# Optimization experiments

Hardware: AMD Instinct MI355X
Metric: run time of the kernel (lower is better)

Reference implementation:

```python
import jax, jax.numpy as jnp
import numpy as np

B, S, D = 2, 2048, 768
H = 12
HD = D // H  # 64
SCALE = HD ** -0.5


def setup_inputs() -> dict:
    key = jax.random.key(0)
    k1, k2, k3, k4, k5 = jax.random.split(key, 5)
    x = jax.random.normal(k1, (B, S, D), dtype=jnp.float32)
    w_qkv = jax.random.normal(k2, (D, 3 * D), dtype=jnp.float32) * (D ** -0.5)
    b_qkv = jax.random.normal(k3, (3 * D,), dtype=jnp.float32) * 0.02
    w_proj = jax.random.normal(k4, (D, D), dtype=jnp.float32) * (D ** -0.5)
    b_proj = jax.random.normal(k5, (D,), dtype=jnp.float32) * 0.02
    return {"x": x, "w_qkv": w_qkv, "b_qkv": b_qkv, "w_proj": w_proj, "b_proj": b_proj}


def reference(x, w_qkv, b_qkv, w_proj, b_proj):
    b, s, d = x.shape
    # QKV projection: (B,S,3D) -> (3,B,H,S,HD)
    qkv = x @ w_qkv + b_qkv
    qkv = qkv.reshape(b, s, 3, H, HD).transpose(2, 0, 3, 1, 4)
    q, k, v = qkv[0], qkv[1], qkv[2]
    q = q * SCALE
    # full NxN attention scores, as in the original module
    attn = jnp.einsum("bhqd,bhkd->bhqk", q, k)
    attn = jax.nn.softmax(attn, axis=-1)
    out = jnp.einsum("bhqk,bhkd->bhqd", attn, v)  # (B,H,S,HD)
    out = out.transpose(0, 2, 1, 3).reshape(b, s, d)
    return out @ w_proj + b_proj
```

## Files before the change

### kernel.cpp

```cpp
#include <hip/hip_runtime.h>
#include <hip/hip_bf16.h>

#define B_ 2
#define S_ 2048
#define D_ 768
#define H_ 12
#define HD_ 64
#define EXP2C_ 0.1803368801111244f

typedef __attribute__((ext_vector_type(8))) short bf16x8;
typedef __attribute__((ext_vector_type(8))) unsigned short u16x8;
typedef __attribute__((ext_vector_type(4))) float f32x4;
typedef __attribute__((ext_vector_type(4))) unsigned int u32x4;

static __device__ __forceinline__ unsigned short f2bf(float x) {
    union { float f; unsigned u; } v; v.f = x;
    unsigned r = (v.u + 0x7FFFu + ((v.u >> 16) & 1u)) >> 16;
    return (unsigned short)r;
}
static __device__ __forceinline__ float bf2f(unsigned short h) {
    union { unsigned u; float f; } v; v.u = ((unsigned)h) << 16;
    return v.f;
}
static __device__ __forceinline__ float fexp2(float x) { return __builtin_exp2f(x); }

static __device__ __forceinline__ unsigned pk_bf16(float a, float b) {
    __hip_bfloat162 pk = __float22bfloat162_rn(make_float2(a, b));
    union { __hip_bfloat162 h; unsigned u; } v; v.h = pk;
    return v.u;
}

static __device__ __forceinline__ f32x4 mfma32(bf16x8 a, bf16x8 b, f32x4 c) {
    return __builtin_amdgcn_mfma_f32_16x16x32_bf16(a, b, c, 0, 0, 0);
}

typedef __attribute__((address_space(3))) unsigned int lds_u32;
typedef __attribute__((address_space(1))) const unsigned int glb_u32;
static __device__ __forceinline__ void glds16(const unsigned short* g, unsigned short* l) {
    __builtin_amdgcn_global_load_lds((glb_u32*)g, (lds_u32*)l, 16, 0, 0);
}

#define PREP_CONV_ 1536
#define PREP_TQKV_ 1728
#define PREP_TPRJ_ 576
__global__ __launch_bounds__(256) void prep_kernel(
    const float* __restrict__ x,      unsigned short* __restrict__ x16,
    const float* __restrict__ w_qkv,  unsigned short* __restrict__ wqkvT,
    const float* __restrict__ w_proj, unsigned short* __restrict__ wprojT)
{
    __shared__ float tile[32][33];
    const int bid = blockIdx.x, t = threadIdx.x;
    if (bid < PREP_CONV_) {
        const int i = (bid * 256 + t) * 8;
        float4 a0 = *(const float4*)(x + i);
        float4 a1 = *(const float4*)(x + i + 4);
        u16x8 s;
        s[0] = f2bf(a0.x); s[1] = f2bf(a0.y); s[2] = f2bf(a0.z); s[3] = f2bf(a0.w);
        s[4] = f2bf(a1.x); s[5] = f2bf(a1.y); s[6] = f2bf(a1.z); s[7] = f2bf(a1.w);
        *(u16x8*)(x16 + i) = s;
        return;
    }
    const float* w; unsigned short* wT; int N, bb;
    if (bid < PREP_CONV_ + PREP_TQKV_) { w = w_qkv; wT = wqkvT; N = 3 * D_; bb = bid - PREP_CONV_; }
    else                               { w = w_proj; wT = wprojT; N = D_;   bb = bid - PREP_CONV_ - PREP_TQKV_; }
    const int K = D_;
    const int nt = N / 32;
    const int n0 = (bb % nt) * 32, k0 = (bb / nt) * 32;
    const int tx = t & 31, ty = t >> 5;
#pragma unroll
    for (int i = 0; i < 4; i++)
        tile[ty + i * 8][tx] = w[(size_t)(k0 + ty + i * 8) * N + n0 + tx];
    __syncthreads();
#pragma unroll
    for (int i = 0; i < 4; i++)
        wT[(size_t)(n0 + ty + i * 8) * K + k0 + tx] = f2bf(tile[tx][ty + i * 8]);
}

template <int BM, int BN, bool OUT_F32>
__global__ __launch_bounds__(256) void gemm_bt_kernel(
    const unsigned short* __restrict__ A,
    const unsigned short* __restrict__ Bt,
    const float* __restrict__ bias,
    void* __restrict__ Cp,
    int M, int N, int K)
{
    __shared__ __align__(16) unsigned short As[BM][32];
    __shared__ __align__(16) unsigned short Bs[BN][32];
    constexpr int MI = BM / 32, NJ = BN / 32;
    constexpr int ACH = BM * 4, BCH = BN * 4;

    const int t = threadIdx.x;
    const int w = t >> 6, lane = t & 63, quad = lane >> 4, l16 = lane & 15;
    const int n0 = blockIdx.x * BN, m0 = blockIdx.y * BM;
    const int mw = (w & 1) * (BM / 2), nw = (w >> 1) * (BN / 2);

    const f32x4 z = {0.f, 0.f, 0.f, 0.f};
    f32x4 acc[MI][NJ];
#pragma unroll
    for (int i = 0; i < MI; i++)
#pragma unroll
        for (int j = 0; j < NJ; j++) acc[i][j] = z;

    for (int kk = 0; kk < K; kk += 32) {
#pragma unroll
        for (int it = 0; it < (ACH + 255) / 256; it++) {
            const int c = t + it * 256;
            if (ACH % 256 == 0 || c < ACH) {
                const int row = c >> 2, c8 = (c & 3) << 3;
                glds16(A + (size_t)(m0 + row) * K + kk + c8, &As[0][0] + c * 8);
            }
        }
#pragma unroll
        for (int it = 0; it < (BCH + 255) / 256; it++) {
            const int c = t + it * 256;
            if (BCH % 256 == 0 || c < BCH) {
                const int row = c >> 2, c8 = (c & 3) << 3;
                glds16(Bt + (size_t)(n0 + row) * K + kk + c8, &Bs[0][0] + c * 8);
            }
        }
        __syncthreads();

        bf16x8 a[MI], b[NJ];
#pragma unroll
        for (int i = 0; i < MI; i++)
            a[i] = *(const bf16x8*)(&As[mw + i * 16 + l16][quad * 8]);
#pragma unroll
        for (int j = 0; j < NJ; j++)
            b[j] = *(const bf16x8*)(&Bs[nw + j * 16 + l16][quad * 8]);
#pragma unroll
        for (int i = 0; i < MI; i++)
#pragma unroll
            for (int j = 0; j < NJ; j++)
                acc[i][j] = mfma32(a[i], b[j], acc[i][j]);
        __syncthreads();
    }

#pragma unroll
    for (int j = 0; j < NJ; j++) {
        const int col = n0 + nw + j * 16 + l16;
        const float bv = bias[col];
#pragma unroll
        for (int i = 0; i < MI; i++) {
#pragma unroll
            for (int r = 0; r < 4; r++) {
                const int row = m0 + mw + i * 16 + quad * 4 + r;
                const float v = acc[i][j][r] + bv;
                if (OUT_F32) ((float*)Cp)[(size_t)row * N + col] = v;
                else         ((unsigned short*)Cp)[(size_t)row * N + col] = f2bf(v);
            }
        }
    }
}

__global__ __launch_bounds__(256) void repack_v_kernel(
    const unsigned short* __restrict__ qkv,
    unsigned short* __restrict__ vt)
{
    __shared__ unsigned short T[64][65];
    const int t = threadIdx.x;
    const int bh = blockIdx.x, st = blockIdx.y;
    const int b = bh / H_, h = bh % H_;
    const unsigned short* src =
        qkv + (size_t)(b * S_ + st * 64) * (3 * D_) + 2 * D_ + h * HD_;

#pragma unroll
    for (int it = 0; it < 2; it++) {
        const int c = t + it * 256, sr = c >> 3, g = c & 7;
        u16x8 v = *(const u16x8*)(src + (size_t)sr * (3 * D_) + g * 8);
#pragma unroll
        for (int j = 0; j < 8; j++) T[sr][g * 8 + j] = v[j];
    }
    __syncthreads();
#pragma unroll
    for (int it = 0; it < 2; it++) {
        const int c = t + it * 256, hd = c >> 3, g = c & 7;
        u16x8 v;
#pragma unroll
        for (int j = 0; j < 8; j++) v[j] = T[g * 8 + j][hd];
        *(u16x8*)(vt + (size_t)(bh * HD_ + hd) * S_ + st * 64 + g * 8) = v;
    }
}

__global__ __launch_bounds__(256) void attn_kernel(
    const unsigned short* __restrict__ qkv,
    const unsigned short* __restrict__ vt,
    float* __restrict__ o_p0,
    float* __restrict__ o_p1,
    float* __restrict__ l_p)
{
    __shared__ __align__(16) unsigned short Ks[2][64][64];
    __shared__ __align__(16) unsigned short Vs[2][64][64];

    const int t = threadIdx.x;
    const int w = t >> 6, lane = t & 63, quad = lane >> 4, l16 = lane & 15;
    const int h8 = l16 & 7;
    const int qt = blockIdx.x, bh = blockIdx.y, ks = blockIdx.z;
    const int b = bh / H_, h = bh % H_;
    const int ld = 3 * D_;

    const unsigned short* qbase =
        qkv + (size_t)(b * S_ + qt * 64 + 16 * w + l16) * ld + h * HD_;
    u16x8 qr0 = *(const u16x8*)(qbase + quad * 8);
    u16x8 qr1 = *(const u16x8*)(qbase + 32 + quad * 8);
    bf16x8 qf0, qf1;
#pragma unroll
    for (int j = 0; j < 8; j++) {
        qf0[j] = (short)f2bf(bf2f(qr0[j]) * EXP2C_);
        qf1[j] = (short)f2bf(bf2f(qr1[j]) * EXP2C_);
    }

    bf16x8 ones;
#pragma unroll
    for (int j = 0; j < 8; j++) ones[j] = (short)0x3F80;

    const unsigned short* kbase =
        qkv + (size_t)(b * S_ + ks * 1024) * ld + D_ + h * HD_;
    const unsigned short* vbase = vt + (size_t)bh * HD_ * S_;

    const int c0 = t, c1 = t + 256;
    const int row0 = c0 >> 3, row1 = c1 >> 3;
    const int kg0 = (c0 & 7) ^ ((row0 & 3) | (((row0 >> 3) & 1) << 2));
    const int kg1 = (c1 & 7) ^ ((row1 & 3) | (((row1 >> 3) & 1) << 2));
    const int vg0 = (c0 & 7) ^ (row0 & 7);
    const int vg1 = (c1 & 7) ^ (row1 & 7);
    const unsigned short* kp0 = kbase + (size_t)row0 * ld + kg0 * 8;
    const unsigned short* kp1 = kbase + (size_t)row1 * ld + kg1 * 8;
    const unsigned short* vp0 = vbase + (size_t)row0 * S_ + ks * 1024 + vg0 * 8;
    const unsigned short* vp1 = vbase + (size_t)row1 * S_ + ks * 1024 + vg1 * 8;
    const size_t KSTEP = (size_t)64 * ld;

    const f32x4 z = {0.f, 0.f, 0.f, 0.f};
    f32x4 o_acc[4] = {z, z, z, z};
    f32x4 l_acc = z;

    glds16(kp0, &Ks[0][0][0] + c0 * 8);
    glds16(kp1, &Ks[0][0][0] + c1 * 8);
    glds16(vp0, &Vs[0][0][0] + c0 * 8);
    glds16(vp1, &Vs[0][0][0] + c1 * 8);
    kp0 += KSTEP; kp1 += KSTEP; vp0 += 64; vp1 += 64;
    __syncthreads();

    const int NT = 1024 / 64;
    for (int kt = 0; kt < NT; kt++) {
        const int buf = kt & 1;

        if (kt + 1 < NT) {
            unsigned short* kd = &Ks[buf ^ 1][0][0];
            unsigned short* vd = &Vs[buf ^ 1][0][0];
            glds16(kp0, kd + c0 * 8);
            glds16(kp1, kd + c1 * 8);
            glds16(vp0, vd + c0 * 8);
            glds16(vp1, vd + c1 * 8);
            kp0 += KSTEP; kp1 += KSTEP; vp0 += 64; vp1 += 64;
        }

        f32x4 s_acc[4] = {z, z, z, z};
#pragma unroll
        for (int nt = 0; nt < 4; nt++) {
            const int rowp = ((nt >> 1) << 5) + ((l16 >> 2) << 3) + ((nt & 1) << 2) + (l16 & 3);
            const int skr = (rowp & 3) | (((rowp >> 3) & 1) << 2);
            const unsigned short* kr = &Ks[buf][rowp][0];
            bf16x8 k0 = *(const bf16x8*)(kr + (quad ^ skr) * 8);
            bf16x8 k1 = *(const bf16x8*)(kr + ((quad ^ skr) ^ 4) * 8);
            s_acc[nt] = mfma32(k0, qf0, s_acc[nt]);
            s_acc[nt] = mfma32(k1, qf1, s_acc[nt]);
        }

        bf16x8 vr0[4], vr1[4];
#pragma unroll
        for (int nt = 0; nt < 4; nt++) {
            const int row = nt * 16 + l16;
            vr0[nt] = *(const bf16x8*)(&Vs[buf][row][(quad ^ h8) * 8]);
            vr1[nt] = *(const bf16x8*)(&Vs[buf][row][((quad ^ h8) ^ 4) * 8]);
        }

        f32x4 pr[4];
#pragma unroll
        for (int nt = 0; nt < 4; nt++) {
#pragma unroll
            for (int r = 0; r < 4; r++) pr[nt][r] = fexp2(s_acc[nt][r]);
        }
        union { u32x4 u; bf16x8 h; } ca, cb;
        ca.u[0] = pk_bf16(pr[0][0], pr[0][1]);
        ca.u[1] = pk_bf16(pr[0][2], pr[0][3]);
        ca.u[2] = pk_bf16(pr[1][0], pr[1][1]);
        ca.u[3] = pk_bf16(pr[1][2], pr[1][3]);
        cb.u[0] = pk_bf16(pr[2][0], pr[2][1]);
        cb.u[1] = pk_bf16(pr[2][2], pr[2][3]);
        cb.u[2] = pk_bf16(pr[3][0], pr[3][1]);
        cb.u[3] = pk_bf16(pr[3][2], pr[3][3]);
        const bf16x8 pa0 = ca.h, pa1 = cb.h;

        l_acc = mfma32(pa0, ones, l_acc);
        l_acc = mfma32(pa1, ones, l_acc);

#pragma unroll
        for (int nt = 0; nt < 4; nt++) {
            o_acc[nt] = mfma32(pa0, vr0[nt], o_acc[nt]);
            o_acc[nt] = mfma32(pa1, vr1[nt], o_acc[nt]);
        }

        __syncthreads();
    }

    float* op = ks ? o_p1 : o_p0;
    float* lp2 = l_p + (size_t)ks * (B_ * S_ * H_);
#pragma unroll
    for (int r = 0; r < 4; r++) {
        const int row = b * S_ + qt * 64 + 16 * w + quad * 4 + r;
        float* ob = op + (size_t)row * D_ + h * HD_;
#pragma unroll
        for (int nt = 0; nt < 4; nt++)
            ob[nt * 16 + l16] = o_acc[nt][r];
        if (l16 == 0) lp2[(size_t)row * H_ + h] = l_acc[r];
    }
}

__global__ __launch_bounds__(256) void combine_kernel(
    const float* __restrict__ o_p0,
    const float* __restrict__ o_p1,
    const float* __restrict__ l_p,
    unsigned short* __restrict__ o)
{
    const int i = (blockIdx.x * 256 + threadIdx.x) * 8;
    const int row = i / D_, col = i - row * D_, h = col >> 6;
    const float l0 = l_p[(size_t)row * H_ + h];
    const float l1 = l_p[(size_t)(B_ * S_ * H_) + row * H_ + h];
    const float inv = 1.f / (l0 + l1);
    float4 a0 = *(const float4*)(o_p0 + i);
    float4 a1 = *(const float4*)(o_p0 + i + 4);
    float4 b0 = *(const float4*)(o_p1 + i);
    float4 b1 = *(const float4*)(o_p1 + i + 4);
    u16x8 s;
    s[0] = f2bf((a0.x + b0.x) * inv); s[1] = f2bf((a0.y + b0.y) * inv);
    s[2] = f2bf((a0.z + b0.z) * inv); s[3] = f2bf((a0.w + b0.w) * inv);
    s[4] = f2bf((a1.x + b1.x) * inv); s[5] = f2bf((a1.y + b1.y) * inv);
    s[6] = f2bf((a1.z + b1.z) * inv); s[7] = f2bf((a1.w + b1.w) * inv);
    *(u16x8*)(o + i) = s;
}

extern "C" void kernel_launch(void* const* d_in, const int* in_sizes, int n_in,
                              void* d_out, int out_size, void* d_ws, size_t ws_size,
                              hipStream_t stream) {
    const float* x      = (const float*)d_in[0];
    const float* w_qkv  = (const float*)d_in[1];
    const float* b_qkv  = (const float*)d_in[2];
    const float* w_proj = (const float*)d_in[3];
    const float* b_proj = (const float*)d_in[4];
    float* out = (float*)d_out;

    unsigned short* qkv    = (unsigned short*)d_ws;
    unsigned short* vtb    = qkv    + (size_t)(B_ * S_) * (3 * D_);
    unsigned short* o_x16  = vtb    + (size_t)(B_ * H_) * HD_ * S_;
    unsigned short* wqkvT  = o_x16  + (size_t)(B_ * S_) * D_;
    unsigned short* wprojT = wqkvT  + (size_t)D_ * (3 * D_);
    float* o_p1 = (float*)(wprojT + (size_t)D_ * D_);
    float* l_p  = o_p1 + (size_t)(B_ * S_) * D_;
    float* o_p0 = out;

    dim3 blk(256);
    prep_kernel<<<dim3(PREP_CONV_ + PREP_TQKV_ + PREP_TPRJ_), blk, 0, stream>>>(
        x, o_x16, w_qkv, wqkvT, w_proj, wprojT);
    gemm_bt_kernel<128, 96, false><<<dim3((3 * D_) / 96, (B_ * S_) / 128), blk, 0, stream>>>(
        o_x16, wqkvT, b_qkv, qkv, B_ * S_, 3 * D_, D_);
    repack_v_kernel<<<dim3(B_ * H_, S_ / 64), blk, 0, stream>>>(qkv, vtb);
    attn_kernel<<<dim3(S_ / 64, B_ * H_, 2), blk, 0, stream>>>(qkv, vtb, o_p0, o_p1, l_p);
    combine_kernel<<<dim3((B_ * S_) * D_ / (256 * 8)), blk, 0, stream>>>(
        o_p0, o_p1, l_p, o_x16);
    gemm_bt_kernel<64, 64, true><<<dim3(D_ / 64, (B_ * S_) / 64), blk, 0, stream>>>(
        o_x16, wprojT, b_proj, out, B_ * S_, D_, D_);
}
```

Measured before the change: 176.3 us.

## Pre-swizzle V into MFMA fragment layout and load it directly to registers

The V-repack kernel now writes V in a layout that already matches the MFMA B-operand fragment order. The attention kernel then loads V fragments from global memory straight into registers, prefetched one tile ahead, and no longer stages them through a shared-memory double buffer. This halves LDS use and removes the LDS reads for V, and a launch-bounds hint asks for 5 blocks per CU. In exchange, every wave now reads V from global memory or cache independently instead of sharing one block load, and register pressure rises.

```diff
diff --git a/kernel.cpp b/kernel.cpp
--- a/kernel.cpp
+++ b/kernel.cpp
@@ -154,7 +154,7 @@
 
 __global__ __launch_bounds__(256) void repack_v_kernel(
     const unsigned short* __restrict__ qkv,
-    unsigned short* __restrict__ vt)
+    unsigned short* __restrict__ vtp)
 {
     __shared__ unsigned short T[64][65];
     const int t = threadIdx.x;
@@ -177,23 +177,23 @@
         u16x8 v;
 #pragma unroll
         for (int j = 0; j < 8; j++) v[j] = T[g * 8 + j][hd];
-        *(u16x8*)(vt + (size_t)(bh * HD_ + hd) * S_ + st * 64 + g * 8) = v;
-    }
-}
-
-__global__ __launch_bounds__(256) void attn_kernel(
+        const size_t off =
+            ((((size_t)(bh * 32 + st) * 4 + (hd >> 4)) * 8 + g) * 16 + (hd & 15)) * 8;
+        *(u16x8*)(vtp + off) = v;
+    }
+}
+
+__global__ __launch_bounds__(256, 5) void attn_kernel(
     const unsigned short* __restrict__ qkv,
-    const unsigned short* __restrict__ vt,
+    const unsigned short* __restrict__ vtp,
     float* __restrict__ o_p0,
     float* __restrict__ o_p1,
     float* __restrict__ l_p)
 {
     __shared__ __align__(16) unsigned short Ks[2][64][64];
-    __shared__ __align__(16) unsigned short Vs[2][64][64];
 
     const int t = threadIdx.x;
     const int w = t >> 6, lane = t & 63, quad = lane >> 4, l16 = lane & 15;
-    const int h8 = l16 & 7;
     const int qt = blockIdx.x, bh = blockIdx.y, ks = blockIdx.z;
     const int b = bh / H_, h = bh % H_;
     const int ld = 3 * D_;
@@ -215,18 +215,15 @@
 
     const unsigned short* kbase =
         qkv + (size_t)(b * S_ + ks * 1024) * ld + D_ + h * HD_;
-    const unsigned short* vbase = vt + (size_t)bh * HD_ * S_;
+    const unsigned short* vb =
+        vtp + ((size_t)bh * 32 + ks * 16) * 4096 + quad * 128 + l16 * 8;
 
     const int c0 = t, c1 = t + 256;
     const int row0 = c0 >> 3, row1 = c1 >> 3;
     const int kg0 = (c0 & 7) ^ ((row0 & 3) | (((row0 >> 3) & 1) << 2));
     const int kg1 = (c1 & 7) ^ ((row1 & 3) | (((row1 >> 3) & 1) << 2));
-    const int vg0 = (c0 & 7) ^ (row0 & 7);
-    const int vg1 = (c1 & 7) ^ (row1 & 7);
     const unsigned short* kp0 = kbase + (size_t)row0 * ld + kg0 * 8;
     const unsigned short* kp1 = kbase + (size_t)row1 * ld + kg1 * 8;
-    const unsigned short* vp0 = vbase + (size_t)row0 * S_ + ks * 1024 + vg0 * 8;
-    const unsigned short* vp1 = vbase + (size_t)row1 * S_ + ks * 1024 + vg1 * 8;
     const size_t KSTEP = (size_t)64 * ld;
 
     const f32x4 z = {0.f, 0.f, 0.f, 0.f};
@@ -235,23 +232,26 @@
 
     glds16(kp0, &Ks[0][0][0] + c0 * 8);
     glds16(kp1, &Ks[0][0][0] + c1 * 8);
-    glds16(vp0, &Vs[0][0][0] + c0 * 8);
-    glds16(vp1, &Vs[0][0][0] + c1 * 8);
-    kp0 += KSTEP; kp1 += KSTEP; vp0 += 64; vp1 += 64;
+    kp0 += KSTEP; kp1 += KSTEP;
+    bf16x8 vc0[4], vc1[4];
+#pragma unroll
+    for (int nt = 0; nt < 4; nt++) {
+        vc0[nt] = *(const bf16x8*)(vb + nt * 1024);
+        vc1[nt] = *(const bf16x8*)(vb + nt * 1024 + 512);
+    }
+    vb += 4096;
     __syncthreads();
 
     const int NT = 1024 / 64;
     for (int kt = 0; kt < NT; kt++) {
         const int buf = kt & 1;
-
-        if (kt + 1 < NT) {
+        const bool pre = (kt + 1 < NT);
+
+        if (pre) {
             unsigned short* kd = &Ks[buf ^ 1][0][0];
-            unsigned short* vd = &Vs[buf ^ 1][0][0];
             glds16(kp0, kd + c0 * 8);
             glds16(kp1, kd + c1 * 8);
-            glds16(vp0, vd + c0 * 8);
-            glds16(vp1, vd + c1 * 8);
-            kp0 += KSTEP; kp1 += KSTEP; vp0 += 64; vp1 += 64;
+            kp0 += KSTEP; kp1 += KSTEP;
         }
 
         f32x4 s_acc[4] = {z, z, z, z};
@@ -264,14 +264,6 @@
             bf16x8 k1 = *(const bf16x8*)(kr + ((quad ^ skr) ^ 4) * 8);
             s_acc[nt] = mfma32(k0, qf0, s_acc[nt]);
             s_acc[nt] = mfma32(k1, qf1, s_acc[nt]);
-        }
-
-        bf16x8 vr0[4], vr1[4];
-#pragma unroll
-        for (int nt = 0; nt < 4; nt++) {
-            const int row = nt * 16 + l16;
-            vr0[nt] = *(const bf16x8*)(&Vs[buf][row][(quad ^ h8) * 8]);
-            vr1[nt] = *(const bf16x8*)(&Vs[buf][row][((quad ^ h8) ^ 4) * 8]);
         }
 
         f32x4 pr[4];
@@ -296,8 +288,17 @@
 
 #pragma unroll
         for (int nt = 0; nt < 4; nt++) {
-            o_acc[nt] = mfma32(pa0, vr0[nt], o_acc[nt]);
-            o_acc[nt] = mfma32(pa1, vr1[nt], o_acc[nt]);
+            o_acc[nt] = mfma32(pa0, vc0[nt], o_acc[nt]);
+            o_acc[nt] = mfma32(pa1, vc1[nt], o_acc[nt]);
+        }
+
+        if (pre) {
+#pragma unroll
+            for (int nt = 0; nt < 4; nt++) {
+                vc0[nt] = *(const bf16x8*)(vb + nt * 1024);
+                vc1[nt] = *(const bf16x8*)(vb + nt * 1024 + 512);
+            }
+            vb += 4096;
         }
 
         __syncthreads();
@@ -350,8 +351,8 @@
     float* out = (float*)d_out;
 
     unsigned short* qkv    = (unsigned short*)d_ws;
-    unsigned short* vtb    = qkv    + (size_t)(B_ * S_) * (3 * D_);
-    unsigned short* o_x16  = vtb    + (size_t)(B_ * H_) * HD_ * S_;
+    unsigned short* vtp    = qkv    + (size_t)(B_ * S_) * (3 * D_);
+    unsigned short* o_x16  = vtp    + (size_t)(B_ * H_) * HD_ * S_;
     unsigned short* wqkvT  = o_x16  + (size_t)(B_ * S_) * D_;
     unsigned short* wprojT = wqkvT  + (size_t)D_ * (3 * D_);
     float* o_p1 = (float*)(wprojT + (size_t)D_ * D_);
@@ -363,8 +364,8 @@
         x, o_x16, w_qkv, wqkvT, w_proj, wprojT);
     gemm_bt_kernel<128, 96, false><<<dim3((3 * D_) / 96, (B_ * S_) / 128), blk, 0, stream>>>(
         o_x16, wqkvT, b_qkv, qkv, B_ * S_, 3 * D_, D_);
-    repack_v_kernel<<<dim3(B_ * H_, S_ / 64), blk, 0, stream>>>(qkv, vtb);
-    attn_kernel<<<dim3(S_ / 64, B_ * H_, 2), blk, 0, stream>>>(qkv, vtb, o_p0, o_p1, l_p);
+    repack_v_kernel<<<dim3(B_ * H_, S_ / 64), blk, 0, stream>>>(qkv, vtp);
+    attn_kernel<<<dim3(S_ / 64, B_ * H_, 2), blk, 0, stream>>>(qkv, vtp, o_p0, o_p1, l_p);
     combine_kernel<<<dim3((B_ * S_) * D_ / (256 * 8)), blk, 0, stream>>>(
         o_p0, o_p1, l_p, o_x16);
     gemm_bt_kernel<64, 64, true><<<dim3(D_ / 64, (B_ * S_) / 64), blk, 0, stream>>>(
```

Result: slower. 181.3 us (+2.8%).

## Fuse split-K attention combine into output projection GEMM A-tile load

Applied to the files above, without the earlier changes.

Removes the separate combine kernel. The projection GEMM now reads both fp32 partial attention outputs, normalizes them by the summed softmax denominators, converts to bf16 and stores the result straight into the shared-memory A tile. This drops one launch and the bf16 intermediate round-trip through global memory. In exchange, each of the 12 column blocks re-reads the fp32 partials (twice the bytes of bf16), and the A loads are synchronous with no prefetch. o_p0 is moved into workspace because out is now the GEMM output.

```diff
diff --git a/kernel.cpp b/kernel.cpp
--- a/kernel.cpp
+++ b/kernel.cpp
@@ -316,27 +316,87 @@
     }
 }
 
-__global__ __launch_bounds__(256) void combine_kernel(
+__global__ __launch_bounds__(256) void gemm2_fused_kernel(
     const float* __restrict__ o_p0,
     const float* __restrict__ o_p1,
     const float* __restrict__ l_p,
-    unsigned short* __restrict__ o)
+    const unsigned short* __restrict__ Bt,
+    const float* __restrict__ bias,
+    float* __restrict__ out)
 {
-    const int i = (blockIdx.x * 256 + threadIdx.x) * 8;
-    const int row = i / D_, col = i - row * D_, h = col >> 6;
-    const float l0 = l_p[(size_t)row * H_ + h];
-    const float l1 = l_p[(size_t)(B_ * S_ * H_) + row * H_ + h];
-    const float inv = 1.f / (l0 + l1);
-    float4 a0 = *(const float4*)(o_p0 + i);
-    float4 a1 = *(const float4*)(o_p0 + i + 4);
-    float4 b0 = *(const float4*)(o_p1 + i);
-    float4 b1 = *(const float4*)(o_p1 + i + 4);
-    u16x8 s;
-    s[0] = f2bf((a0.x + b0.x) * inv); s[1] = f2bf((a0.y + b0.y) * inv);
-    s[2] = f2bf((a0.z + b0.z) * inv); s[3] = f2bf((a0.w + b0.w) * inv);
-    s[4] = f2bf((a1.x + b1.x) * inv); s[5] = f2bf((a1.y + b1.y) * inv);
-    s[6] = f2bf((a1.z + b1.z) * inv); s[7] = f2bf((a1.w + b1.w) * inv);
-    *(u16x8*)(o + i) = s;
+    __shared__ __align__(16) unsigned short As[64][32];
+    __shared__ __align__(16) unsigned short Bs[64][32];
+    __shared__ float linv[64 * 13];
+
+    const int t = threadIdx.x;
+    const int w = t >> 6, lane = t & 63, quad = lane >> 4, l16 = lane & 15;
+    const int n0 = blockIdx.x * 64, m0 = blockIdx.y * 64;
+    const int mw = (w & 1) * 32, nw = (w >> 1) * 32;
+
+    for (int i = t; i < 64 * H_; i += 256) {
+        const int row = i / H_, hh = i - row * H_;
+        const float l0 = l_p[(size_t)(m0 + row) * H_ + hh];
+        const float l1 = l_p[(size_t)(B_ * S_ * H_) + (size_t)(m0 + row) * H_ + hh];
+        linv[row * 13 + hh] = 1.f / (l0 + l1);
+    }
+
+    const f32x4 z = {0.f, 0.f, 0.f, 0.f};
+    f32x4 acc[2][2];
+#pragma unroll
+    for (int i = 0; i < 2; i++)
+#pragma unroll
+        for (int j = 0; j < 2; j++) acc[i][j] = z;
+
+    const int arow = t >> 2, ac8 = (t & 3) << 3;
+    const float* ap0 = o_p0 + (size_t)(m0 + arow) * D_ + ac8;
+    const float* ap1 = o_p1 + (size_t)(m0 + arow) * D_ + ac8;
+    const unsigned short* bp = Bt + (size_t)(n0 + arow) * D_ + ac8;
+
+    __syncthreads();
+
+    for (int kk = 0; kk < D_; kk += 32) {
+        const float4 a0 = *(const float4*)(ap0 + kk);
+        const float4 a1 = *(const float4*)(ap0 + kk + 4);
+        const float4 b0 = *(const float4*)(ap1 + kk);
+        const float4 b1 = *(const float4*)(ap1 + kk + 4);
+        glds16(bp + kk, &Bs[0][0] + t * 8);
+        const float inv = linv[arow * 13 + (kk >> 6)];
+        u16x8 s;
+        s[0] = f2bf((a0.x + b0.x) * inv); s[1] = f2bf((a0.y + b0.y) * inv);
+        s[2] = f2bf((a0.z + b0.z) * inv); s[3] = f2bf((a0.w + b0.w) * inv);
+        s[4] = f2bf((a1.x + b1.x) * inv); s[5] = f2bf((a1.y + b1.y) * inv);
+        s[6] = f2bf((a1.z + b1.z) * inv); s[7] = f2bf((a1.w + b1.w) * inv);
+        *(u16x8*)(&As[0][0] + t * 8) = s;
+        __syncthreads();
+
+        bf16x8 a[2], b[2];
+#pragma unroll
+        for (int i = 0; i < 2; i++)
+            a[i] = *(const bf16x8*)(&As[mw + i * 16 + l16][quad * 8]);
+#pragma unroll
+        for (int j = 0; j < 2; j++)
+            b[j] = *(const bf16x8*)(&Bs[nw + j * 16 + l16][quad * 8]);
+#pragma unroll
+        for (int i = 0; i < 2; i++)
+#pragma unroll
+            for (int j = 0; j < 2; j++)
+                acc[i][j] = mfma32(a[i], b[j], acc[i][j]);
+        __syncthreads();
+    }
+
+#pragma unroll
+    for (int j = 0; j < 2; j++) {
+        const int col = n0 + nw + j * 16 + l16;
+        const float bv = bias[col];
+#pragma unroll
+        for (int i = 0; i < 2; i++) {
+#pragma unroll
+            for (int r = 0; r < 4; r++) {
+                const int row = m0 + mw + i * 16 + quad * 4 + r;
+                out[(size_t)row * D_ + col] = acc[i][j][r] + bv;
+            }
+        }
+    }
 }
 
 extern "C" void kernel_launch(void* const* d_in, const int* in_sizes, int n_in,
@@ -351,22 +411,20 @@
 
     unsigned short* qkv    = (unsigned short*)d_ws;
     unsigned short* vtb    = qkv    + (size_t)(B_ * S_) * (3 * D_);
-    unsigned short* o_x16  = vtb    + (size_t)(B_ * H_) * HD_ * S_;
-    unsigned short* wqkvT  = o_x16  + (size_t)(B_ * S_) * D_;
+    unsigned short* x16    = vtb    + (size_t)(B_ * H_) * HD_ * S_;
+    unsigned short* wqkvT  = x16    + (size_t)(B_ * S_) * D_;
     unsigned short* wprojT = wqkvT  + (size_t)D_ * (3 * D_);
     float* o_p1 = (float*)(wprojT + (size_t)D_ * D_);
     float* l_p  = o_p1 + (size_t)(B_ * S_) * D_;
-    float* o_p0 = out;
+    float* o_p0 = l_p + (size_t)2 * B_ * S_ * H_;
 
     dim3 blk(256);
     prep_kernel<<<dim3(PREP_CONV_ + PREP_TQKV_ + PREP_TPRJ_), blk, 0, stream>>>(
-        x, o_x16, w_qkv, wqkvT, w_proj, wprojT);
+        x, x16, w_qkv, wqkvT, w_proj, wprojT);
     gemm_bt_kernel<128, 96, false><<<dim3((3 * D_) / 96, (B_ * S_) / 128), blk, 0, stream>>>(
-        o_x16, wqkvT, b_qkv, qkv, B_ * S_, 3 * D_, D_);
+        x16, wqkvT, b_qkv, qkv, B_ * S_, 3 * D_, D_);
     repack_v_kernel<<<dim3(B_ * H_, S_ / 64), blk, 0, stream>>>(qkv, vtb);
     attn_kernel<<<dim3(S_ / 64, B_ * H_, 2), blk, 0, stream>>>(qkv, vtb, o_p0, o_p1, l_p);
-    combine_kernel<<<dim3((B_ * S_) * D_ / (256 * 8)), blk, 0, stream>>>(
-        o_p0, o_p1, l_p, o_x16);
-    gemm_bt_kernel<64, 64, true><<<dim3(D_ / 64, (B_ * S_) / 64), blk, 0, stream>>>(
-        o_x16, wprojT, b_proj, out, B_ * S_, D_, D_);
-}
+    gemm2_fused_kernel<<<dim3(D_ / 64, (B_ * S_) / 64), blk, 0, stream>>>(
+        o_p0, o_p1, l_p, wprojT, b_proj, out);
+}
```

Measured after the change: 189.7 us. +7.6%, slower.

## Deepen GEMM K-tile to 64 with XOR-swizzled LDS; raise wave priority around attention MFMAs

Applied to the files above, without the earlier changes.

The bf16 GEMM kernel now stages a 64-wide K slice per iteration instead of 32. That halves the number of barrier-separated load/compute rounds, and an XOR swizzle of the 16-byte chunks avoids LDS bank conflicts on the wider rows. Separately, the attention inner loop wraps its QK and PV MFMA blocks in s_setprio(1)/s_setprio(0) so that waves issuing matrix work get scheduling priority over waves doing loads and exp. The larger tile doubles LDS use per block, which may reduce occupancy.

```diff
diff --git a/kernel.cpp b/kernel.cpp
--- a/kernel.cpp
+++ b/kernel.cpp
@@ -84,10 +84,12 @@
     void* __restrict__ Cp,
     int M, int N, int K)
 {
-    __shared__ __align__(16) unsigned short As[BM][32];
-    __shared__ __align__(16) unsigned short Bs[BN][32];
+    constexpr int BK = 64;
+    __shared__ __align__(16) unsigned short As[BM][BK];
+    __shared__ __align__(16) unsigned short Bs[BN][BK];
     constexpr int MI = BM / 32, NJ = BN / 32;
-    constexpr int ACH = BM * 4, BCH = BN * 4;
+    constexpr int ACH = BM * BK / 8;
+    constexpr int BCH = BN * BK / 8;
 
     const int t = threadIdx.x;
     const int w = t >> 6, lane = t & 63, quad = lane >> 4, l16 = lane & 15;
@@ -101,37 +103,42 @@
 #pragma unroll
         for (int j = 0; j < NJ; j++) acc[i][j] = z;
 
-    for (int kk = 0; kk < K; kk += 32) {
-#pragma unroll
-        for (int it = 0; it < (ACH + 255) / 256; it++) {
+    for (int kk = 0; kk < K; kk += BK) {
+#pragma unroll
+        for (int it = 0; it < ACH / 256; it++) {
             const int c = t + it * 256;
-            if (ACH % 256 == 0 || c < ACH) {
-                const int row = c >> 2, c8 = (c & 3) << 3;
-                glds16(A + (size_t)(m0 + row) * K + kk + c8, &As[0][0] + c * 8);
+            const int row = c >> 3, gs = (c & 7) ^ (row & 7);
+            glds16(A + (size_t)(m0 + row) * K + kk + gs * 8, &As[0][0] + c * 8);
+        }
+#pragma unroll
+        for (int it = 0; it < BCH / 256; it++) {
+            const int c = t + it * 256;
+            const int row = c >> 3, gs = (c & 7) ^ (row & 7);
+            glds16(Bt + (size_t)(n0 + row) * K + kk + gs * 8, &Bs[0][0] + c * 8);
+        }
+        __syncthreads();
+
+#pragma unroll
+        for (int k2 = 0; k2 < 2; k2++) {
+            bf16x8 a[MI], b[NJ];
+#pragma unroll
+            for (int i = 0; i < MI; i++) {
+                const int row = mw + i * 16 + l16;
+                const int p = (quad + k2 * 4) ^ (row & 7);
+                a[i] = *(const bf16x8*)(&As[row][p * 8]);
             }
-        }
-#pragma unroll
-        for (int it = 0; it < (BCH + 255) / 256; it++) {
-            const int c = t + it * 256;
-            if (BCH % 256 == 0 || c < BCH) {
-                const int row = c >> 2, c8 = (c & 3) << 3;
-                glds16(Bt + (size_t)(n0 + row) * K + kk + c8, &Bs[0][0] + c * 8);
+#pragma unroll
+            for (int j = 0; j < NJ; j++) {
+                const int row = nw + j * 16 + l16;
+                const int p = (quad + k2 * 4) ^ (row & 7);
+                b[j] = *(const bf16x8*)(&Bs[row][p * 8]);
             }
-        }
-        __syncthreads();
-
-        bf16x8 a[MI], b[NJ];
-#pragma unroll
-        for (int i = 0; i < MI; i++)
-            a[i] = *(const bf16x8*)(&As[mw + i * 16 + l16][quad * 8]);
-#pragma unroll
-        for (int j = 0; j < NJ; j++)
-            b[j] = *(const bf16x8*)(&Bs[nw + j * 16 + l16][quad * 8]);
-#pragma unroll
-        for (int i = 0; i < MI; i++)
-#pragma unroll
-            for (int j = 0; j < NJ; j++)
-                acc[i][j] = mfma32(a[i], b[j], acc[i][j]);
+#pragma unroll
+            for (int i = 0; i < MI; i++)
+#pragma unroll
+                for (int j = 0; j < NJ; j++)
+                    acc[i][j] = mfma32(a[i], b[j], acc[i][j]);
+        }
         __syncthreads();
     }
 
@@ -255,6 +262,7 @@
         }
 
         f32x4 s_acc[4] = {z, z, z, z};
+        __builtin_amdgcn_s_setprio(1);
 #pragma unroll
         for (int nt = 0; nt < 4; nt++) {
             const int rowp = ((nt >> 1) << 5) + ((l16 >> 2) << 3) + ((nt & 1) << 2) + (l16 & 3);
@@ -265,6 +273,7 @@
             s_acc[nt] = mfma32(k0, qf0, s_acc[nt]);
             s_acc[nt] = mfma32(k1, qf1, s_acc[nt]);
         }
+        __builtin_amdgcn_s_setprio(0);
 
         bf16x8 vr0[4], vr1[4];
 #pragma unroll
@@ -291,14 +300,15 @@
         cb.u[3] = pk_bf16(pr[3][2], pr[3][3]);
         const bf16x8 pa0 = ca.h, pa1 = cb.h;
 
+        __builtin_amdgcn_s_setprio(1);
         l_acc = mfma32(pa0, ones, l_acc);
         l_acc = mfma32(pa1, ones, l_acc);
-
 #pragma unroll
         for (int nt = 0; nt < 4; nt++) {
             o_acc[nt] = mfma32(pa0, vr0[nt], o_acc[nt]);
             o_acc[nt] = mfma32(pa1, vr1[nt], o_acc[nt]);
         }
+        __builtin_amdgcn_s_setprio(0);
 
         __syncthreads();
     }
```

Result: faster. 171.2 us (-2.9%).
